# Kernel tuning notes

Hardware: AMD Instinct MI355X
Metric: run time of the kernel (lower is better)

The kernel has to match this reference:

```python
import jax, jax.numpy as jnp
import numpy as np

B, S, T, H, NH, G, E, I, R, L = 256, 256, 16, 1024, 8, 3, 8, 4096, 256, 3
GTEMP, RTEMP, TOPK_G, NEG = 1.0, 1.0, 2, -1e9

_W = {
    'ts_in_w': (3*H, H), 'ts_out_w': (H, H),
    'st_in_w': (3*H, H), 'st_out_w': (H, H),
    'ca_in_w': (3*H, H), 'ca_out_w': (H, H),
    'opq_w': (H, H), 'fuse_w': (H, 3*H), 'gate_w': (H, 3*H),
    'bs_w': (R, H), 'bt_w': (R, H), 'bo_w': (H, R),
    'cond_w': (H, 2*H), 'gr_w': (G, H), 'er_w': (G, E, H),
    'e_w1': (G, E, I, H), 'e_w2': (G, E, H, I), 'cls_w': (L, H),
}
_B = {
    'ts_in_b': (3*H,), 'ts_out_b': (H,), 'st_in_b': (3*H,), 'st_out_b': (H,),
    'ca_in_b': (3*H,), 'ca_out_b': (H,), 'fuse_b': (H,), 'gate_b': (H,),
    'bs_b': (R,), 'bt_b': (R,), 'bo_b': (H,), 'cond_b': (H,),
    'gr_b': (G,), 'er_b': (G, E), 'e_b1': (G, E, I), 'e_b2': (G, E, H),
    'cls_b': (L,), 'ln_b': (3*H,),
}


def setup_inputs() -> dict:
    key = jax.random.key(0)
    out = {}
    out['h_sent'] = jax.random.normal(jax.random.fold_in(key, 1), (B, S, H), dtype=jnp.float32)
    out['h_term'] = jax.random.normal(jax.random.fold_in(key, 2), (B, T, H), dtype=jnp.float32)
    for i, (name, shp) in enumerate(_W.items()):
        out[name] = 0.02 * jax.random.normal(jax.random.fold_in(key, 100 + i), shp, dtype=jnp.float32)
    for name, shp in _B.items():
        out[name] = jnp.zeros(shp, dtype=jnp.float32)
    out['ln_g'] = jnp.ones((3*H,), dtype=jnp.float32)
    return out


def _mha(q, k, v, w_in, b_in, w_out, b_out):
    # torch nn.MultiheadAttention (batch_first, eval mode / no dropout)
    wq, wk, wv = jnp.split(w_in, 3, axis=0)
    bq, bk, bv = jnp.split(b_in, 3, axis=0)
    Q, K, V = q @ wq.T + bq, k @ wk.T + bk, v @ wv.T + bv
    b, lq, _ = Q.shape
    lk = K.shape[1]
    d = H // NH
    Q = Q.reshape(b, lq, NH, d).transpose(0, 2, 1, 3)
    K = K.reshape(b, lk, NH, d).transpose(0, 2, 1, 3)
    V = V.reshape(b, lk, NH, d).transpose(0, 2, 1, 3)
    att = jax.nn.softmax(jnp.einsum('bhqd,bhkd->bhqk', Q, K) * (1.0 / d ** 0.5), axis=-1)
    o = jnp.einsum('bhqk,bhkd->bhqd', att, V).transpose(0, 2, 1, 3).reshape(b, lq, H)
    return o @ w_out.T + b_out


def _ln(x, g, b, eps=1e-5):
    mu = x.mean(-1, keepdims=True)
    var = ((x - mu) ** 2).mean(-1, keepdims=True)
    return (x - mu) * jax.lax.rsqrt(var + eps) * g + b


def reference(h_sent, h_term, ts_in_w, ts_in_b, ts_out_w, ts_out_b,
              st_in_w, st_in_b, st_out_w, st_out_b,
              ca_in_w, ca_in_b, ca_out_w, ca_out_b,
              opq_w, ln_g, ln_b, fuse_w, fuse_b, gate_w, gate_b,
              bs_w, bs_b, bt_w, bt_b, bo_w, bo_b, cond_w, cond_b,
              gr_w, gr_b, er_w, er_b, e_w1, e_b1, e_w2, e_b2, cls_w, cls_b):
    # --- co-attention fusion ---
    t2s = _mha(h_term, h_sent, h_sent, ts_in_w, ts_in_b, ts_out_w, ts_out_b)  # [B,T,H]
    s2t = _mha(h_sent, h_term, h_term, st_in_w, st_in_b, st_out_w, st_out_b)  # [B,S,H]
    v_term = t2s.mean(axis=1)   # [B,H]
    v_sent = s2t.mean(axis=1)   # [B,H]
    oq = h_term @ opq_w.T       # opinion query projection (no bias)
    v_op = _mha(oq, h_sent, h_sent, ca_in_w, ca_in_b, ca_out_w, ca_out_b).mean(axis=1)
    cat3 = jnp.concatenate([v_sent, v_term, v_op], axis=-1)        # [B,3H]
    fused_lin = _ln(cat3, ln_g, ln_b) @ fuse_w.T + fuse_b           # [B,H]
    g = jax.nn.sigmoid(cat3 @ gate_w.T + gate_b)                    # [B,H]
    bil = ((v_sent @ bs_w.T + bs_b) * (v_term @ bt_w.T + bt_b)) @ bo_w.T + bo_b
    fused = g * fused_lin + (1.0 - g) * bil                         # [B,H]
    cond = jnp.concatenate([fused, v_term], axis=-1) @ cond_w.T + cond_b  # [B,H]
    # --- hierarchical group -> expert soft routing ---
    glog = fused @ gr_w.T + gr_b                                    # [B,G]
    thr = jax.lax.top_k(glog, TOPK_G)[0][:, -1:]
    glog = jnp.where(glog >= thr, glog, NEG)
    gp = jax.nn.softmax(glog / GTEMP, axis=-1)                      # [B,G]
    elog = jnp.einsum('bh,geh->bge', cond, er_w) + er_b             # [B,G,E]
    ep = jax.nn.softmax(elog / RTEMP, axis=-1)
    # all experts applied densely (soft routing); FFN experts: GELU MLP
    h1 = jax.nn.gelu(jnp.einsum('bh,geih->bgei', fused, e_w1) + e_b1, approximate=False)
    y = jnp.einsum('bgei,gehi->bgeh', h1, e_w2) + e_b2              # [B,G,E,H]
    moe = jnp.einsum('bge,bgeh->bh', gp[:, :, None] * ep, y)
    out = fused + moe                                               # residual merge
    return out @ cls_w.T + cls_b                                    # [B,L]
```

## Files before the change

kernel.cpp:

```cpp
#include <hip/hip_runtime.h>
#include <math.h>


#define B_    256
#define S_    256
#define T_    16
#define H_    1024
#define NH_   8
#define DH_   128
#define M128_ 128
#define G_    3
#define E_    8
#define I_    4096
#define R_    256
#define L_    3
#define GE_   24

using bf16x8 = __attribute__((ext_vector_type(8))) __bf16;
using f32x4  = __attribute__((ext_vector_type(4))) float;

__device__ inline float wave_sum(float v) {
    for (int o = 32; o > 0; o >>= 1) v += __shfl_xor(v, o);
    return v;
}
__device__ inline float wave_max(float v) {
    for (int o = 32; o > 0; o >>= 1) v = fmaxf(v, __shfl_xor(v, o));
    return v;
}

__device__ inline void split8(const float4& f0, const float4& f1, bf16x8& hi, bf16x8& lo)
{
    const float fv[8] = {f0.x, f0.y, f0.z, f0.w, f1.x, f1.y, f1.z, f1.w};
#pragma unroll
    for (int j = 0; j < 8; ++j) {
        const __bf16 h = (__bf16)fv[j];
        hi[j] = h; lo[j] = (__bf16)(fv[j] - (float)h);
    }
}

__global__ __launch_bounds__(512) void fsc_k(
    const float* __restrict__ QALL, const float* __restrict__ wT3,
    const float* __restrict__ hs, const float* __restrict__ OFFS3,
    float* __restrict__ SC3, float rscale)
{
    const int zz = ((blockIdx.z & 7) << 7) | (blockIdx.z >> 3);
    const int b = zz >> 2, mod = zz & 3;
    if (mod == 3) return;

    __shared__ __bf16 A64h[128 * 72];
    __shared__ __bf16 A64l[128 * 72];
    __shared__ __bf16 Bh[128 * 40];
    __shared__ __bf16 Bl[128 * 40];

    const int tid  = threadIdx.x;
    const int lane = tid & 63;
    const int wid  = tid >> 6;
    const int fr   = lane & 15;
    const int fk   = lane >> 4;
    const int wm2  = (wid >> 2) * 64;
    const int wn2  = (wid & 3) * 32;

    bf16x8 qh[4], ql[4];
    {
        const float* qb = QALL + ((long)(b * 16 + fr)) * 4096 + mod * 1024 + wid * 128;
#pragma unroll
        for (int jc = 0; jc < 4; ++jc) {
            const float* p = qb + jc * 32 + fk * 8;
            split8(*(const float4*)p, *(const float4*)(p + 4), qh[jc], ql[jc]);
        }
    }

    f32x4 acc[2][4][2] = {};
    const float* wbase = wT3 + (long)mod * 1048576 + wid * 128;
    const float* hb = hs + (long)b * 262144;

    for (int ks = 0; ks < 16; ++ks) {
        __syncthreads();
#pragma unroll
        for (int nt = 0; nt < 4; ++nt) {
            f32x4 pa = {};
            const float* wr = wbase + (long)(ks * 64 + nt * 16 + fr) * 1024;
#pragma unroll
            for (int jc = 0; jc < 4; ++jc) {
                const float* p = wr + jc * 32 + fk * 8;
                bf16x8 wh, wl;
                split8(*(const float4*)p, *(const float4*)(p + 4), wh, wl);
                pa = __builtin_amdgcn_mfma_f32_16x16x32_bf16(qh[jc], wh, pa, 0, 0, 0);
                pa = __builtin_amdgcn_mfma_f32_16x16x32_bf16(qh[jc], wl, pa, 0, 0, 0);
                pa = __builtin_amdgcn_mfma_f32_16x16x32_bf16(ql[jc], wh, pa, 0, 0, 0);
            }
            const int kl = nt * 16 + fr;
#pragma unroll
            for (int r = 0; r < 4; ++r) {
                const int m = (fk * 4 + r) * 8 + wid;
                const float v = pa[r];
                const __bf16 hv = (__bf16)v;
                A64h[m * 72 + kl] = hv;
                A64l[m * 72 + kl] = (__bf16)(v - (float)hv);
            }
        }
#pragma unroll
        for (int half = 0; half < 2; ++half) {
#pragma unroll
            for (int kc = 0; kc < 2; ++kc) {
                __syncthreads();
                {
                    const int r2 = tid >> 2, q2 = tid & 3;
                    const float* p = hb + (long)(half * 128 + r2) * 1024 +
                                     ks * 64 + kc * 32 + q2 * 8;
                    bf16x8 hh, hl;
                    split8(*(const float4*)p, *(const float4*)(p + 4), hh, hl);
                    *(bf16x8*)&Bh[r2 * 40 + q2 * 8] = hh;
                    *(bf16x8*)&Bl[r2 * 40 + q2 * 8] = hl;
                }
                __syncthreads();
                const int klo = kc * 32 + fk * 8;
#pragma unroll
                for (int mt = 0; mt < 4; ++mt) {
                    const bf16x8 ah = *(const bf16x8*)&A64h[(wm2 + mt * 16 + fr) * 72 + klo];
                    const bf16x8 al = *(const bf16x8*)&A64l[(wm2 + mt * 16 + fr) * 72 + klo];
#pragma unroll
                    for (int nt = 0; nt < 2; ++nt) {
                        const bf16x8 bh = *(const bf16x8*)&Bh[(wn2 + nt * 16 + fr) * 40 + fk * 8];
                        const bf16x8 bl = *(const bf16x8*)&Bl[(wn2 + nt * 16 + fr) * 40 + fk * 8];
                        acc[half][mt][nt] = __builtin_amdgcn_mfma_f32_16x16x32_bf16(ah, bh, acc[half][mt][nt], 0, 0, 0);
                        acc[half][mt][nt] = __builtin_amdgcn_mfma_f32_16x16x32_bf16(ah, bl, acc[half][mt][nt], 0, 0, 0);
                        acc[half][mt][nt] = __builtin_amdgcn_mfma_f32_16x16x32_bf16(al, bh, acc[half][mt][nt], 0, 0, 0);
                    }
                }
            }
        }
    }

    float* out = SC3 + (long)mod * 8388608 + (long)b * 32768;
    const float* ro = OFFS3 + mod * 32768 + b * 128;
    const int lr4 = fk * 4;
#pragma unroll
    for (int half = 0; half < 2; ++half)
#pragma unroll
        for (int mt = 0; mt < 4; ++mt)
#pragma unroll
            for (int r = 0; r < 4; ++r) {
                const int rr = wm2 + mt * 16 + lr4 + r;
                const float rov = ro[rr];
#pragma unroll
                for (int nt = 0; nt < 2; ++nt) {
                    const int cc = half * 128 + wn2 + nt * 16 + fr;
                    out[(long)rr * 256 + cc] = (acc[half][mt][nt][r] + rov) * rscale;
                }
            }
}

template <int ACT>
__global__ __launch_bounds__(256) void sgemm2_k(
    const float* __restrict__ Ap, const float* __restrict__ Bp,
    const float* __restrict__ biasp, const float* __restrict__ roffp,
    float* __restrict__ Cf,
    int K, int m2shift, int zshift,
    long sA1, long sA2, long sAz1, long sAz2,
    long ldb, long sBz1, long sBz2, long sBia1, long sBia2,
    long sC1, long sC2, long sCz1, long sCz2, long sR1, long sR2,
    float scale)
{
    const int z  = blockIdx.z;
    const int z1 = z >> zshift;
    const int z2 = z & ((1 << zshift) - 1);
    const int m2mask = (1 << m2shift) - 1;
    const int row0 = blockIdx.y * 128;
    const int col0 = blockIdx.x * 128;
    const float* Ab = Ap + (long)z1 * sAz1 + (long)z2 * sAz2;
    const float* Bb = Bp + (long)z1 * sBz1 + (long)z2 * sBz2;
    const float* biasb = biasp ? biasp + (long)z1 * sBia1 + (long)z2 * sBia2 : nullptr;
    const float* roffb = roffp ? roffp + (long)z1 * sR1 + (long)z2 * sR2 : nullptr;

    __shared__ __bf16 Ahs[128 * 40];
    __shared__ __bf16 Als[128 * 40];
    __shared__ __bf16 Bhs[128 * 40];
    __shared__ __bf16 Bls[128 * 40];

    const int tid  = threadIdx.x;
    const int lane = tid & 63;
    const int wid  = tid >> 6;
    const int wm = (wid >> 1) * 64;
    const int wn = (wid & 1) * 64;
    const int fr  = lane & 15;
    const int fkb = (lane >> 4) * 16;
    const int qrow = tid >> 2;
    const int c4   = tid & 3;

    f32x4 acc[4][4] = {};
    float4 pfa[2][2], pfb[2][2];

    auto loadAB = [&](int k0) {
#pragma unroll
        for (int rep = 0; rep < 2; ++rep) {
            const int row = qrow + rep * 64;
            const int r = row0 + row;
            const int r1 = r >> m2shift, r2 = r & m2mask;
            const float* srcA = Ab + (long)r1 * sA1 + (long)r2 * sA2 + k0 + c4 * 8;
            pfa[rep][0] = *(const float4*)srcA;
            pfa[rep][1] = *(const float4*)(srcA + 4);
            const float* srcB = Bb + (long)(col0 + row) * ldb + k0 + c4 * 8;
            pfb[rep][0] = *(const float4*)srcB;
            pfb[rep][1] = *(const float4*)(srcB + 4);
        }
    };

    loadAB(0);
    for (int k0 = 0; k0 < K; k0 += 32) {
        __syncthreads();
#pragma unroll
        for (int rep = 0; rep < 2; ++rep) {
            const int row = qrow + rep * 64;
            bf16x8 hi, lo;
            split8(pfa[rep][0], pfa[rep][1], hi, lo);
            *(bf16x8*)&Ahs[row * 40 + c4 * 8] = hi;
            *(bf16x8*)&Als[row * 40 + c4 * 8] = lo;
            split8(pfb[rep][0], pfb[rep][1], hi, lo);
            *(bf16x8*)&Bhs[row * 40 + c4 * 8] = hi;
            *(bf16x8*)&Bls[row * 40 + c4 * 8] = lo;
        }
        __syncthreads();
        if (k0 + 32 < K) loadAB(k0 + 32);

        bf16x8 bh4[4], bl4[4];
#pragma unroll
        for (int n = 0; n < 4; ++n) {
            bh4[n] = *(const bf16x8*)((const char*)&Bhs[(wn + n * 16 + fr) * 40] + fkb);
            bl4[n] = *(const bf16x8*)((const char*)&Bls[(wn + n * 16 + fr) * 40] + fkb);
        }
#pragma unroll
        for (int m = 0; m < 4; ++m) {
            const bf16x8 ah = *(const bf16x8*)((const char*)&Ahs[(wm + m * 16 + fr) * 40] + fkb);
            const bf16x8 al = *(const bf16x8*)((const char*)&Als[(wm + m * 16 + fr) * 40] + fkb);
#pragma unroll
            for (int n = 0; n < 4; ++n) {
                acc[m][n] = __builtin_amdgcn_mfma_f32_16x16x32_bf16(ah, bh4[n], acc[m][n], 0, 0, 0);
                acc[m][n] = __builtin_amdgcn_mfma_f32_16x16x32_bf16(ah, bl4[n], acc[m][n], 0, 0, 0);
                acc[m][n] = __builtin_amdgcn_mfma_f32_16x16x32_bf16(al, bh4[n], acc[m][n], 0, 0, 0);
            }
        }
    }

    float* Cfb = Cf + (long)z1 * sCz1 + (long)z2 * sCz2;
    const int lr4 = (lane >> 4) * 4;
#pragma unroll
    for (int m = 0; m < 4; ++m) {
#pragma unroll
        for (int r = 0; r < 4; ++r) {
            const int rr = row0 + wm + m * 16 + lr4 + r;
            const int r1 = rr >> m2shift, r2 = rr & m2mask;
            const float ro = roffb ? roffb[rr] : 0.f;
            const long cb = (long)r1 * sC1 + (long)r2 * sC2;
#pragma unroll
            for (int n = 0; n < 4; ++n) {
                const int cc = col0 + wn + n * 16 + fr;
                float v = (acc[m][n][r] + ro) * scale;
                if (biasp) v += biasb[cc];
                if (ACT == 2) v = 1.0f / (1.0f + expf(-v));
                Cfb[cb + cc] = v;
            }
        }
    }
}

static void sg2(hipStream_t s, int act,
                const float* A, const float* B, const float* bias, const float* roff,
                float* C, int gx, int gy, int gz,
                int K, int m2shift, int zshift,
                long sA1, long sA2, long sAz1, long sAz2,
                long ldb, long sBz1, long sBz2, long sBia1, long sBia2,
                long sC1, long sC2, long sCz1, long sCz2, long sR1, long sR2,
                float scale)
{
    dim3 g(gx, gy, gz), b(256);
#define S2ARGS A, B, bias, roff, C, K, m2shift, zshift, sA1, sA2, sAz1, sAz2, \
               ldb, sBz1, sBz2, sBia1, sBia2, sC1, sC2, sCz1, sCz2, sR1, sR2, scale
    if (act == 2) sgemm2_k<2><<<g, b, 0, s>>>(S2ARGS);
    else          sgemm2_k<0><<<g, b, 0, s>>>(S2ARGS);
#undef S2ARGS
}

template <int ABF16, int BSING, int ACT, int WMUL, int OUTH>
__global__ __launch_bounds__(512) void sgemm256_k(
    const void* __restrict__ Ap, const float* __restrict__ Bp,
    const float* __restrict__ biasp, const float* __restrict__ wmulp,
    float* __restrict__ Cf, __bf16* __restrict__ Ch,
    int K, long sA1, long sAz, long ldb, long sBz, long sBz2, int bzshift,
    long sBias, long sC1, long sCz, long sWr, float scale)
{
    const int z    = blockIdx.z;
    const int col0 = blockIdx.x * 128;
    const int z1 = z >> bzshift;
    const int z2 = z - (z1 << bzshift);
    const float* Bb = Bp + (long)z1 * sBz + (long)z2 * sBz2;
    const float* biasb = biasp ? biasp + (long)z1 * sBias : nullptr;

    __shared__ __bf16 Ah[256 * 40];
    __shared__ __bf16 Al[ABF16 ? 64 : 256 * 40];
    __shared__ __bf16 Bh[128 * 40];
    __shared__ __bf16 Bl[BSING ? 64 : 128 * 40];

    const int tid  = threadIdx.x;
    const int lane = tid & 63;
    const int wid  = tid >> 6;
    const int wm = (wid >> 1) * 64;
    const int wn = (wid & 1) * 64;
    const int fr  = lane & 15;
    const int fkb = (lane >> 4) * 16;

    f32x4 acc[4][4] = {};
    bf16x8 pfah[2];
    float4 pfaf[2][2];
    float4 pfb[2];

    auto loadAB = [&](int k0) {
#pragma unroll
        for (int rep = 0; rep < 2; ++rep) {
            const int idx = tid + rep * 512;
            const int row = idx >> 2;
            const int cc4 = idx & 3;
            if (ABF16) {
                pfah[rep] = *(const bf16x8*)((const __bf16*)Ap + (long)z * sAz +
                                             (long)row * sA1 + k0 + cc4 * 8);
            } else {
                const float* src = (const float*)Ap + (long)z * sAz +
                                   (long)row * sA1 + k0 + cc4 * 8;
                pfaf[rep][0] = *(const float4*)src;
                pfaf[rep][1] = *(const float4*)(src + 4);
            }
        }
        {
            const int row = tid >> 2;
            const int cc4 = tid & 3;
            const float* src = Bb + (long)(col0 + row) * ldb + k0 + cc4 * 8;
            pfb[0] = *(const float4*)src;
            pfb[1] = *(const float4*)(src + 4);
        }
    };

    loadAB(0);
    for (int k0 = 0; k0 < K; k0 += 32) {
        __syncthreads();
#pragma unroll
        for (int rep = 0; rep < 2; ++rep) {
            const int idx = tid + rep * 512;
            const int row = idx >> 2;
            const int cc4 = idx & 3;
            if (ABF16) {
                *(bf16x8*)&Ah[row * 40 + cc4 * 8] = pfah[rep];
            } else {
                bf16x8 hi, lo;
                split8(pfaf[rep][0], pfaf[rep][1], hi, lo);
                *(bf16x8*)&Ah[row * 40 + cc4 * 8] = hi;
                *(bf16x8*)&Al[row * 40 + cc4 * 8] = lo;
            }
        }
        {
            const int row = tid >> 2;
            const int cc4 = tid & 3;
            bf16x8 hi, lo;
            split8(pfb[0], pfb[1], hi, lo);
            *(bf16x8*)&Bh[row * 40 + cc4 * 8] = hi;
            if (!BSING) *(bf16x8*)&Bl[row * 40 + cc4 * 8] = lo;
        }
        __syncthreads();
        if (k0 + 32 < K) loadAB(k0 + 32);

        bf16x8 bh4[4], bl4[4];
#pragma unroll
        for (int n = 0; n < 4; ++n) {
            bh4[n] = *(const bf16x8*)((const char*)&Bh[(wn + n * 16 + fr) * 40] + fkb);
            if (!BSING) bl4[n] = *(const bf16x8*)((const char*)&Bl[(wn + n * 16 + fr) * 40] + fkb);
        }
#pragma unroll
        for (int m = 0; m < 4; ++m) {
            const bf16x8 ah = *(const bf16x8*)((const char*)&Ah[(wm + m * 16 + fr) * 40] + fkb);
            bf16x8 al;
            if (!ABF16) al = *(const bf16x8*)((const char*)&Al[(wm + m * 16 + fr) * 40] + fkb);
#pragma unroll
            for (int n = 0; n < 4; ++n) {
                acc[m][n] = __builtin_amdgcn_mfma_f32_16x16x32_bf16(ah, bh4[n], acc[m][n], 0, 0, 0);
                if (!BSING) acc[m][n] = __builtin_amdgcn_mfma_f32_16x16x32_bf16(ah, bl4[n], acc[m][n], 0, 0, 0);
                if (!ABF16) acc[m][n] = __builtin_amdgcn_mfma_f32_16x16x32_bf16(al, bh4[n], acc[m][n], 0, 0, 0);
            }
        }
    }

    const int lr4 = (lane >> 4) * 4;
#pragma unroll
    for (int m = 0; m < 4; ++m) {
#pragma unroll
        for (int r = 0; r < 4; ++r) {
            const int rr = wm + m * 16 + lr4 + r;
#pragma unroll
            for (int n = 0; n < 4; ++n) {
                const int cc = col0 + wn + n * 16 + fr;
                float v = acc[m][n][r] * scale;
                if (biasp) v += biasb[cc];
                if (ACT == 1) v = 0.5f * v * (1.0f + erff(v * 0.70710678118654752f));
                if (WMUL) v *= wmulp[(long)rr * sWr + z];
                if (OUTH) Ch[(long)z * sCz + (long)rr * sC1 + cc] = (__bf16)v;
                else      Cf[(long)z * sCz + (long)rr * sC1 + cc] = v;
            }
        }
    }
}

__global__ void dotk_k(const float* __restrict__ A, const float* __restrict__ Bw,
                       const float* __restrict__ bias, float* __restrict__ out,
                       int MN, int N, int K)
{
    const int idx = blockIdx.x * (blockDim.x >> 6) + (threadIdx.x >> 6);
    if (idx >= MN) return;
    const int m = idx / N, n = idx - m * N;
    const int lane = threadIdx.x & 63;
    const float* a = A + (long)m * K;
    const float* bb = Bw + (long)n * K;
    float s = 0.f;
    for (int k = lane * 4; k < K; k += 256) {
        const float4 av = *(const float4*)(a + k);
        const float4 bv = *(const float4*)(bb + k);
        s += av.x * bv.x + av.y * bv.y + av.z * bv.z + av.w * bv.w;
    }
    s = wave_sum(s);
    if (lane == 0) out[idx] = s + (bias ? bias[n] : 0.f);
}

template <int ACT>
__global__ void kred_k(const float* __restrict__ part, const float* __restrict__ bias,
                       float* __restrict__ out, int n, long stride, int nz, int biasMask)
{
    const int i = blockIdx.x * blockDim.x + threadIdx.x;
    if (i >= n) return;
    float v = 0.f;
    for (int z = 0; z < nz; ++z) v += part[(long)z * stride + i];
    if (bias) v += bias[i & biasMask];
    if (ACT == 2) v = 1.0f / (1.0f + expf(-v));
    out[i] = v;
}

__global__ void cpy8_k(const float* s0, const float* s1, const float* s2, const float* s3,
                       const float* s4, const float* s5, const float* s6, const float* s7,
                       float* d0, float* d1, float* d2, float* d3,
                       float* d4, float* d5, float* d6, float* d7)
{
    const int seg = blockIdx.x >> 10;
    const int i = ((blockIdx.x & 1023) * 256 + threadIdx.x);
    const float* srcs[8] = {s0, s1, s2, s3, s4, s5, s6, s7};
    float* dsts[8] = {d0, d1, d2, d3, d4, d5, d6, d7};
    ((float4*)dsts[seg])[i] = ((const float4*)srcs[seg])[i];
}

__global__ void tT4_k(const float* s0, const float* s1, const float* s2, const float* s3,
                      float* d0, float* d1, float* d2, float* d3)
{
    __shared__ float t[32][33];
    const int seg = blockIdx.y >> 5;
    const float* src = seg == 0 ? s0 : seg == 1 ? s1 : seg == 2 ? s2 : s3;
    float* dst = seg == 0 ? d0 : seg == 1 ? d1 : seg == 2 ? d2 : d3;
    const int c0 = blockIdx.x * 32, r0 = (blockIdx.y & 31) * 32;
    const int tx = threadIdx.x & 31, ty = threadIdx.x >> 5;
#pragma unroll
    for (int i = 0; i < 4; ++i) {
        const int r = ty + i * 8;
        t[r][tx] = src[(long)(r0 + r) * 1024 + c0 + tx];
    }
    __syncthreads();
#pragma unroll
    for (int i = 0; i < 4; ++i) {
        const int r = ty + i * 8;
        dst[(long)(c0 + r) * 1024 + r0 + tx] = t[tx][r];
    }
}

__global__ void biascat_k(const float* __restrict__ ts_b, const float* __restrict__ ca_b,
                          const float* __restrict__ st_b,
                          const float* __restrict__ ts_ob, const float* __restrict__ ca_ob,
                          const float* __restrict__ st_ob,
                          float* __restrict__ BCAT, float* __restrict__ BKCAT,
                          float* __restrict__ WVB, float* __restrict__ WOB)
{
    const int i = blockIdx.x * blockDim.x + threadIdx.x;
    if (i >= 1024) return;
    BCAT[i] = ts_b[i]; BCAT[1024 + i] = ca_b[i];
    BCAT[2048 + i] = st_b[1024 + i]; BCAT[3072 + i] = st_b[2048 + i];
    BKCAT[i] = ts_b[1024 + i]; BKCAT[1024 + i] = ca_b[1024 + i]; BKCAT[2048 + i] = st_b[i];
    WVB[i] = ts_b[2048 + i]; WVB[1024 + i] = ca_b[2048 + i];
    WOB[i] = ts_ob[i]; WOB[1024 + i] = ca_ob[i]; WOB[2048 + i] = st_ob[i];
}

__global__ void headdot3_k(const float* __restrict__ QALL, const float* __restrict__ BKCAT,
                           float* __restrict__ out)
{
    const int idx = blockIdx.x * blockDim.x + threadIdx.x;
    if (idx >= 3 * B_ * T_ * NH_) return;
    const int mod = idx >> 15;
    const int b = (idx >> 7) & 255;
    const int t = (idx >> 3) & 15;
    const int h = idx & 7;
    const float* q = QALL + (long)(b * 16 + t) * 4096 + mod * 1024 + h * 128;
    const float* bb = BKCAT + mod * 1024 + h * 128;
    float sum = 0.f;
    for (int k = 0; k < DH_; ++k) sum += q[k] * bb[k];
    out[idx] = sum;
}

__global__ __launch_bounds__(64) void softpb_k(const float* __restrict__ sc3,
                                               float* __restrict__ pbar,
                                               float* __restrict__ attm)
{
    const int blk = blockIdx.x;
    const int h = blk & 7;
    const int b = (blk >> 3) & 255;
    const int mod = blk >> 11;
    const int lane = threadIdx.x;
    const float* base = sc3 + (long)mod * 8388608 + (long)b * 32768 + (long)h * 256;
    float v[16][4];
#pragma unroll
    for (int t = 0; t < 16; ++t) {
        const float* rowp = base + (long)t * 2048;
#pragma unroll
        for (int j = 0; j < 4; ++j) v[t][j] = rowp[j * 64 + lane];
    }
    if (mod < 2) {
        float pb[4] = {0.f, 0.f, 0.f, 0.f};
#pragma unroll
        for (int t = 0; t < 16; ++t) {
            float m = fmaxf(fmaxf(v[t][0], v[t][1]), fmaxf(v[t][2], v[t][3]));
            m = wave_max(m);
            const float e0 = expf(v[t][0] - m), e1 = expf(v[t][1] - m);
            const float e2 = expf(v[t][2] - m), e3 = expf(v[t][3] - m);
            const float inv = 1.f / wave_sum(e0 + e1 + e2 + e3);
            pb[0] += e0 * inv; pb[1] += e1 * inv; pb[2] += e2 * inv; pb[3] += e3 * inv;
        }
        float* pd = pbar + (long)mod * 524288 + (long)b * 2048 + h * 256;
#pragma unroll
        for (int j = 0; j < 4; ++j) pd[j * 64 + lane] = pb[j] * (1.0f / 16.f);
    } else {
        float am[16];
#pragma unroll
        for (int t = 0; t < 16; ++t) am[t] = 0.f;
#pragma unroll
        for (int j = 0; j < 4; ++j) {
            float mx = v[0][j];
#pragma unroll
            for (int t = 1; t < 16; ++t) mx = fmaxf(mx, v[t][j]);
            float e[16];
            float sum = 0.f;
#pragma unroll
            for (int t = 0; t < 16; ++t) { e[t] = expf(v[t][j] - mx); sum += e[t]; }
            const float inv = 1.f / sum;
#pragma unroll
            for (int t = 0; t < 16; ++t) am[t] += e[t] * inv;
        }
#pragma unroll
        for (int t = 0; t < 16; ++t) {
            const float sm = wave_sum(am[t]) * (1.0f / 256.f);
            if (lane == 0) attm[b * 128 + t * 8 + h] = sm;
        }
    }
}

__global__ __launch_bounds__(256) void ctxw2_k(const float* __restrict__ pbar,
                                               const float* __restrict__ hs,
                                               float* __restrict__ part)
{
    const int b = blockIdx.x;
    const int sc = blockIdx.y;
    __shared__ float pl[16][64];
    const int tid = threadIdx.x;
    for (int i = tid; i < 16 * 64; i += 256) {
        const int row = i >> 6;
        const int mod = row >> 3;
        pl[row][i & 63] = pbar[(long)mod * 524288 + (long)b * 2048 +
                               (row & 7) * 256 + sc * 64 + (i & 63)];
    }
    __syncthreads();
    const int k0 = tid * 4;
    float4 acc[16] = {};
    const float* hb = hs + (long)b * S_ * H_ + (long)sc * 64 * H_;
    for (int s = 0; s < 64; ++s) {
        const float4 vv = *(const float4*)(hb + (long)s * H_ + k0);
#pragma unroll
        for (int j = 0; j < 16; ++j) {
            const float p = pl[j][s];
            acc[j].x += p * vv.x; acc[j].y += p * vv.y;
            acc[j].z += p * vv.z; acc[j].w += p * vv.w;
        }
    }
    float* ob = part + (long)sc * 4194304;
#pragma unroll
    for (int j = 0; j < 16; ++j) {
        const int mod = j >> 3, hh = j & 7;
        *(float4*)(ob + (long)mod * 2097152 + (long)b * 8192 + hh * 1024 + k0) = acc[j];
    }
}

__global__ void ohead2_k(const float* __restrict__ attm, const float* __restrict__ QALL,
                         float* __restrict__ outb)
{
    const int idx = blockIdx.x * blockDim.x + threadIdx.x;
    if (idx >= B_ * H_) return;
    const int c = idx & (H_ - 1);
    const int b = idx >> 10;
    float sv = 0.f;
#pragma unroll
    for (int t = 0; t < T_; ++t)
        sv += attm[b * M128_ + t * NH_ + (c >> 7)] * QALL[(long)(b * 16 + t) * 4096 + 3072 + c];
    outb[idx] = sv;
}

__global__ void cat3_k(const float* __restrict__ vs, const float* __restrict__ vt,
                       const float* __restrict__ vo, float* __restrict__ out)
{
    const int idx = blockIdx.x * blockDim.x + threadIdx.x;
    if (idx >= B_ * 3 * H_) return;
    const int k = idx % (3 * H_);
    const int b = idx / (3 * H_);
    float v;
    if (k < H_)          v = vs[b * H_ + k];
    else if (k < 2 * H_) v = vt[b * H_ + k - H_];
    else                 v = vo[b * H_ + k - 2 * H_];
    out[idx] = v;
}

__global__ void ln_k(const float* __restrict__ cat3, const float* __restrict__ g,
                     const float* __restrict__ bta, float* __restrict__ out)
{
    const int b = blockIdx.x;
    const int tid = threadIdx.x;
    __shared__ float buf[3 * H_];
    __shared__ float red[4];
    const float* src = cat3 + (long)b * 3 * H_;
    float sv = 0.f;
    for (int i = tid; i < 3 * H_; i += 256) { const float x = src[i]; buf[i] = x; sv += x; }
    sv = wave_sum(sv);
    if ((tid & 63) == 0) red[tid >> 6] = sv;
    __syncthreads();
    const float mu = (red[0] + red[1] + red[2] + red[3]) * (1.f / (3 * H_));
    __syncthreads();
    float s2 = 0.f;
    for (int i = tid; i < 3 * H_; i += 256) { const float d0 = buf[i] - mu; s2 += d0 * d0; }
    s2 = wave_sum(s2);
    if ((tid & 63) == 0) red[tid >> 6] = s2;
    __syncthreads();
    const float var = (red[0] + red[1] + red[2] + red[3]) * (1.f / (3 * H_));
    const float rstd = rsqrtf(var + 1e-5f);
    float* dst = out + (long)b * 3 * H_;
    for (int i = tid; i < 3 * H_; i += 256)
        dst[i] = (buf[i] - mu) * rstd * g[i] + bta[i];
}

__global__ void mulf_k(const float* __restrict__ a, const float* __restrict__ b2,
                       float* __restrict__ out, int n)
{
    const int idx = blockIdx.x * blockDim.x + threadIdx.x;
    if (idx < n) out[idx] = a[idx] * b2[idx];
}

__global__ void fuse_k(const float* __restrict__ g, const float* __restrict__ flin,
                       const float* __restrict__ bil, float* __restrict__ fused,
                       __bf16* __restrict__ fusedh)
{
    const int idx = blockIdx.x * blockDim.x + threadIdx.x;
    if (idx >= B_ * H_) return;
    const float gg = g[idx];
    const float v = gg * flin[idx] + (1.f - gg) * bil[idx];
    fused[idx] = v;
    fusedh[idx] = (__bf16)v;
}

__global__ void catfv_k(const float* __restrict__ fused, const float* __restrict__ vt,
                        float* __restrict__ out)
{
    const int idx = blockIdx.x * blockDim.x + threadIdx.x;
    if (idx >= B_ * 2 * H_) return;
    const int k = idx % (2 * H_);
    const int b = idx / (2 * H_);
    out[idx] = (k < H_) ? fused[b * H_ + k] : vt[b * H_ + k - H_];
}

__global__ void route_k(const float* __restrict__ glog, float* __restrict__ gp)
{
    const int b = blockIdx.x * blockDim.x + threadIdx.x;
    if (b >= B_) return;
    const float x0 = glog[b * 3], x1 = glog[b * 3 + 1], x2 = glog[b * 3 + 2];
    const float m1 = fmaxf(x0, fmaxf(x1, x2));
    float thr;
    if (x0 == m1)      thr = fmaxf(x1, x2);
    else if (x1 == m1) thr = fmaxf(x0, x2);
    else               thr = fmaxf(x0, x1);
    const float y0 = (x0 >= thr) ? x0 : -1e9f;
    const float y1 = (x1 >= thr) ? x1 : -1e9f;
    const float y2 = (x2 >= thr) ? x2 : -1e9f;
    const float mm = fmaxf(y0, fmaxf(y1, y2));
    const float e0 = expf(y0 - mm), e1 = expf(y1 - mm), e2 = expf(y2 - mm);
    const float inv = 1.f / (e0 + e1 + e2);
    gp[b * 3] = e0 * inv; gp[b * 3 + 1] = e1 * inv; gp[b * 3 + 2] = e2 * inv;
}

__global__ void epsm_k(float* __restrict__ elog, const float* __restrict__ gp)
{
    const int idx = blockIdx.x * blockDim.x + threadIdx.x;
    if (idx >= B_ * G_) return;
    float* p = elog + (long)idx * E_;
    float m = p[0];
#pragma unroll
    for (int e = 1; e < E_; ++e) m = fmaxf(m, p[e]);
    float sum = 0.f;
    float v[E_];
#pragma unroll
    for (int e = 0; e < E_; ++e) { v[e] = expf(p[e] - m); sum += v[e]; }
    const float w = gp[idx] / sum;
#pragma unroll
    for (int e = 0; e < E_; ++e) p[e] = v[e] * w;
}

__global__ void moefinal_k(const float* __restrict__ part, const float* __restrict__ fused,
                           const float* __restrict__ wsc, const float* __restrict__ e_b2,
                           float* __restrict__ res)
{
    const int idx = blockIdx.x * blockDim.x + threadIdx.x;
    if (idx >= B_ * H_) return;
    const int b = idx >> 10;
    const int h = idx & (H_ - 1);
    float acc = fused[idx];
#pragma unroll 8
    for (int z = 0; z < 48; ++z) acc += part[(long)z * (B_ * H_) + idx];
    float ba = 0.f;
#pragma unroll
    for (int ge = 0; ge < GE_; ++ge) ba += wsc[b * GE_ + ge] * e_b2[ge * H_ + h];
    res[idx] = acc + ba;
}

extern "C" void kernel_launch(void* const* d_in, const int* in_sizes, int n_in,
                              void* d_out, int out_size, void* d_ws, size_t ws_size,
                              hipStream_t stream)
{
    const float* h_sent  = (const float*)d_in[0];
    const float* h_term  = (const float*)d_in[1];
    const float* ts_in_w = (const float*)d_in[2];
    const float* ts_out_w= (const float*)d_in[3];
    const float* st_in_w = (const float*)d_in[4];
    const float* st_out_w= (const float*)d_in[5];
    const float* ca_in_w = (const float*)d_in[6];
    const float* ca_out_w= (const float*)d_in[7];
    const float* opq_w   = (const float*)d_in[8];
    const float* fuse_w  = (const float*)d_in[9];
    const float* gate_w  = (const float*)d_in[10];
    const float* bs_w    = (const float*)d_in[11];
    const float* bt_w    = (const float*)d_in[12];
    const float* bo_w    = (const float*)d_in[13];
    const float* cond_w  = (const float*)d_in[14];
    const float* gr_w    = (const float*)d_in[15];
    const float* er_w    = (const float*)d_in[16];
    const float* e_w1    = (const float*)d_in[17];
    const float* e_w2    = (const float*)d_in[18];
    const float* cls_w   = (const float*)d_in[19];
    const float* ts_in_b = (const float*)d_in[20];
    const float* ts_out_b= (const float*)d_in[21];
    const float* st_in_b = (const float*)d_in[22];
    const float* st_out_b= (const float*)d_in[23];
    const float* ca_in_b = (const float*)d_in[24];
    const float* ca_out_b= (const float*)d_in[25];
    const float* fuse_b  = (const float*)d_in[26];
    const float* gate_b  = (const float*)d_in[27];
    const float* bs_b    = (const float*)d_in[28];
    const float* bt_b    = (const float*)d_in[29];
    const float* bo_b    = (const float*)d_in[30];
    const float* cond_b  = (const float*)d_in[31];
    const float* gr_b    = (const float*)d_in[32];
    const float* er_b    = (const float*)d_in[33];
    const float* e_b1    = (const float*)d_in[34];
    const float* e_b2    = (const float*)d_in[35];
    const float* cls_b   = (const float*)d_in[36];
    const float* ln_b    = (const float*)d_in[37];
    const float* ln_g    = (const float*)d_in[38];
    (void)in_sizes; (void)n_in; (void)out_size; (void)ws_size;

    float* ws = (float*)d_ws;
    size_t off = 0;
    auto allocF = [&](size_t n) { float* p = ws + off; off += (n + 63) & ~(size_t)63; return p; };

    float* QALL  = allocF(16777216);
    float* WCAT  = allocF(4194304);
    float* BCAT  = allocF(4096);
    float* BKCAT = allocF(3072);
    float* wT3   = allocF(3145728);
    float* opqT  = allocF(1048576);
    float* WVCAT = allocF(2097152);
    float* WVB   = allocF(2048);
    float* WOCAT = allocF(3145728);
    float* WOB   = allocF(3072);
    float* OFFS3 = allocF(98304);
    float* SC3   = allocF(25165824);
    float* PBAR3 = allocF(1048576);
    float* CTXB3 = allocF(4194304);
    float* PARTC = allocF(16777216);
    float* OBAR3 = allocF(786432);
    float* VOUT3 = allocF(786432);
    float* ATTM  = allocF(32768);
    float* CAT3  = allocF(786432);
    float* LNC   = allocF(786432);
    float* FLIN  = allocF(262144);
    float* GATE  = allocF(262144);
    float* BSV   = allocF(65536);
    float* BTV   = allocF(65536);
    float* PROD  = allocF(65536);
    float* BIL   = allocF(262144);
    float* FUSED = allocF(262144);
    float* FUSEDH= allocF(131072);
    float* CATFV = allocF(524288);
    float* COND  = allocF(262144);
    float* GLOG  = allocF(1024);
    float* GP    = allocF(1024);
    float* ELOG  = allocF(8192);
    float* RES   = allocF(262144);
    float* PARTF = allocF(1048576);
    float* H1Wf  = allocF(12582912);
    float* PART  = allocF(12582912);
    __bf16* FUSEDbf = (__bf16*)FUSEDH;
    __bf16* H1W     = (__bf16*)H1Wf;
    float* VTERM = VOUT3;
    float* VOP   = VOUT3 + 262144;
    float* VSENT = VOUT3 + 524288;

    hipStream_t s = stream;
    const float rscale = 0.08838834764831845f;

    cpy8_k<<<dim3(8 * 1024), dim3(256), 0, s>>>(
        ts_in_w, st_in_w + 1048576, st_in_w + 2097152, ts_in_w + 2097152,
        ca_in_w + 2097152, ts_out_w, ca_out_w, st_out_w,
        WCAT, WCAT + 2097152, WCAT + 3145728, WVCAT,
        WVCAT + 1048576, WOCAT, WOCAT + 1048576, WOCAT + 2097152);
    biascat_k<<<dim3(4), dim3(256), 0, s>>>(ts_in_b, ca_in_b, st_in_b,
                                            ts_out_b, ca_out_b, st_out_b,
                                            BCAT, BKCAT, WVB, WOB);
    tT4_k<<<dim3(32, 128), dim3(256), 0, s>>>(
        ts_in_w + 1048576, ca_in_w + 1048576, st_in_w, opq_w,
        wT3, wT3 + 1048576, wT3 + 2097152, opqT);

    sg2(s, 0, ca_in_w, opqT, nullptr, nullptr, WCAT + 1048576,
        8, 8, 1, 1024, 12, 0, 0, 1024, 0, 0, 1024, 0, 0, 0, 0,
        0, 1024, 0, 0, 0, 0, 1.f);

    sg2(s, 0, h_term, WCAT, BCAT, nullptr, QALL,
        32, 32, 1, 1024, 12, 0, 0, 1024, 0, 0, 1024, 0, 0, 0, 0,
        0, 4096, 0, 0, 0, 0, 1.f);

    headdot3_k<<<dim3(384), dim3(256), 0, s>>>(QALL, BKCAT, OFFS3);

    fsc_k<<<dim3(1, 1, 1024), dim3(512), 0, s>>>(QALL, wT3, h_sent, OFFS3, SC3, rscale);

    softpb_k<<<dim3(3 * B_ * NH_), dim3(64), 0, s>>>(SC3, PBAR3, ATTM);

    ctxw2_k<<<dim3(B_, 4), dim3(256), 0, s>>>(PBAR3, h_sent, PARTC);
    kred_k<0><<<dim3(4194304 / 256), dim3(256), 0, s>>>(PARTC, nullptr, CTXB3,
                                                        4194304, 4194304, 4, 0);
    sg2(s, 0, CTXB3, WVCAT, WVB, nullptr, OBAR3,
        1, 2, 16, 1024, 12, 3,
        0, 8192, 2097152, 1024,
        1024, 1048576, 131072, 1024, 128,
        0, 1024, 262144, 128, 0, 0, 1.f);

    ohead2_k<<<dim3((B_ * H_ + 255) / 256), dim3(256), 0, s>>>(ATTM, QALL, OBAR3 + 524288);

    sg2(s, 0, OBAR3, WOCAT, WOB, nullptr, VOUT3,
        8, 2, 3, 1024, 12, 0,
        0, 1024, 262144, 0,
        1024, 1048576, 0, 1024, 0,
        0, 1024, 262144, 0, 0, 0, 1.f);

    cat3_k<<<dim3((B_ * 3 * H_ + 255) / 256), dim3(256), 0, s>>>(VSENT, VTERM, VOP, CAT3);
    ln_k<<<dim3(B_), dim3(256), 0, s>>>(CAT3, ln_g, ln_b, LNC);
    sg2(s, 0, LNC, fuse_w, nullptr, nullptr, PARTF,
        8, 2, 4, 768, 12, 2, 0, 3072, 0, 768, 3072, 0, 768, 0, 0,
        0, 1024, 0, 262144, 0, 0, 1.f);
    kred_k<0><<<dim3(1024), dim3(256), 0, s>>>(PARTF, fuse_b, FLIN, 262144, 262144, 4, 1023);
    sg2(s, 0, CAT3, gate_w, nullptr, nullptr, PARTF,
        8, 2, 4, 768, 12, 2, 0, 3072, 0, 768, 3072, 0, 768, 0, 0,
        0, 1024, 0, 262144, 0, 0, 1.f);
    kred_k<2><<<dim3(1024), dim3(256), 0, s>>>(PARTF, gate_b, GATE, 262144, 262144, 4, 1023);
    sg2(s, 0, VSENT, bs_w, nullptr, nullptr, PARTF,
        2, 2, 4, 256, 12, 2, 0, 1024, 0, 256, 1024, 0, 256, 0, 0,
        0, 256, 0, 65536, 0, 0, 1.f);
    kred_k<0><<<dim3(256), dim3(256), 0, s>>>(PARTF, bs_b, BSV, 65536, 65536, 4, 255);
    sg2(s, 0, VTERM, bt_w, nullptr, nullptr, PARTF,
        2, 2, 4, 256, 12, 2, 0, 1024, 0, 256, 1024, 0, 256, 0, 0,
        0, 256, 0, 65536, 0, 0, 1.f);
    kred_k<0><<<dim3(256), dim3(256), 0, s>>>(PARTF, bt_b, BTV, 65536, 65536, 4, 255);
    mulf_k<<<dim3((B_ * R_ + 255) / 256), dim3(256), 0, s>>>(BSV, BTV, PROD, B_ * R_);
    sg2(s, 0, PROD, bo_w, nullptr, nullptr, PARTF,
        8, 2, 2, 128, 12, 1, 0, 256, 0, 128, 256, 0, 128, 0, 0,
        0, 1024, 0, 262144, 0, 0, 1.f);
    kred_k<0><<<dim3(1024), dim3(256), 0, s>>>(PARTF, bo_b, BIL, 262144, 262144, 2, 1023);
    fuse_k<<<dim3((B_ * H_ + 255) / 256), dim3(256), 0, s>>>(GATE, FLIN, BIL, FUSED, FUSEDbf);
    catfv_k<<<dim3((B_ * 2 * H_ + 255) / 256), dim3(256), 0, s>>>(FUSED, VTERM, CATFV);
    sg2(s, 0, CATFV, cond_w, nullptr, nullptr, PARTF,
        8, 2, 4, 512, 12, 2, 0, 2048, 0, 512, 2048, 0, 512, 0, 0,
        0, 1024, 0, 262144, 0, 0, 1.f);
    kred_k<0><<<dim3(1024), dim3(256), 0, s>>>(PARTF, cond_b, COND, 262144, 262144, 4, 1023);

    dotk_k<<<dim3(192), dim3(256), 0, s>>>(FUSED, gr_w, gr_b, GLOG, B_ * G_, G_, H_);
    route_k<<<dim3(1), dim3(256), 0, s>>>(GLOG, GP);
    dotk_k<<<dim3(1536), dim3(256), 0, s>>>(COND, er_w, er_b, ELOG, B_ * GE_, GE_, H_);
    epsm_k<<<dim3(3), dim3(256), 0, s>>>(ELOG, GP);

    sgemm256_k<1, 1, 1, 1, 1><<<dim3(I_ / 128, 1, GE_), dim3(512), 0, s>>>(
        FUSEDbf, e_w1, e_b1, ELOG, nullptr, H1W,
        1024, H_, 0, H_, (long)I_ * H_, 0, 0, I_,
        (long)GE_ * I_, I_, GE_, 1.f);
    sgemm256_k<1, 1, 0, 0, 0><<<dim3(H_ / 128, 1, 2 * GE_), dim3(512), 0, s>>>(
        H1W, e_w2, nullptr, nullptr, PART, nullptr,
        2048, (long)GE_ * I_, 2048, I_, (long)H_ * I_, 2048, 1, 0,
        H_, (long)B_ * H_, 0, 1.f);
    moefinal_k<<<dim3(B_ * H_ / 256), dim3(256), 0, s>>>(PART, FUSED, ELOG, e_b2, RES);

    dotk_k<<<dim3(192), dim3(256), 0, s>>>(RES, cls_w, cls_b, (float*)d_out, B_ * L_, L_, H_);
}
```

Baseline: 1.764 ms.

## Replace fused score kernel with two generic GEMMs through an intermediate buffer

Removes the fused fsc_k kernel, which projected queries through the key weights and multiplied by h_sent within one block using split-bf16 MFMA. It now runs two sgemm2 launches: the first writes per-head query-key products into a large BIG3 workspace, and the second multiplies that by h_sent with the offset and scale applied. This reuses the tuned generic GEMM and drops the awkward fused staging with its many barriers. In exchange it writes and re-reads an intermediate of roughly 400MB in global memory.

```diff
diff --git a/kernel.cpp b/kernel.cpp
--- a/kernel.cpp
+++ b/kernel.cpp
@@ -36,119 +36,6 @@
         const __bf16 h = (__bf16)fv[j];
         hi[j] = h; lo[j] = (__bf16)(fv[j] - (float)h);
     }
-}
-
-__global__ __launch_bounds__(512) void fsc_k(
-    const float* __restrict__ QALL, const float* __restrict__ wT3,
-    const float* __restrict__ hs, const float* __restrict__ OFFS3,
-    float* __restrict__ SC3, float rscale)
-{
-    const int zz = ((blockIdx.z & 7) << 7) | (blockIdx.z >> 3);
-    const int b = zz >> 2, mod = zz & 3;
-    if (mod == 3) return;
-
-    __shared__ __bf16 A64h[128 * 72];
-    __shared__ __bf16 A64l[128 * 72];
-    __shared__ __bf16 Bh[128 * 40];
-    __shared__ __bf16 Bl[128 * 40];
-
-    const int tid  = threadIdx.x;
-    const int lane = tid & 63;
-    const int wid  = tid >> 6;
-    const int fr   = lane & 15;
-    const int fk   = lane >> 4;
-    const int wm2  = (wid >> 2) * 64;
-    const int wn2  = (wid & 3) * 32;
-
-    bf16x8 qh[4], ql[4];
-    {
-        const float* qb = QALL + ((long)(b * 16 + fr)) * 4096 + mod * 1024 + wid * 128;
-#pragma unroll
-        for (int jc = 0; jc < 4; ++jc) {
-            const float* p = qb + jc * 32 + fk * 8;
-            split8(*(const float4*)p, *(const float4*)(p + 4), qh[jc], ql[jc]);
-        }
-    }
-
-    f32x4 acc[2][4][2] = {};
-    const float* wbase = wT3 + (long)mod * 1048576 + wid * 128;
-    const float* hb = hs + (long)b * 262144;
-
-    for (int ks = 0; ks < 16; ++ks) {
-        __syncthreads();
-#pragma unroll
-        for (int nt = 0; nt < 4; ++nt) {
-            f32x4 pa = {};
-            const float* wr = wbase + (long)(ks * 64 + nt * 16 + fr) * 1024;
-#pragma unroll
-            for (int jc = 0; jc < 4; ++jc) {
-                const float* p = wr + jc * 32 + fk * 8;
-                bf16x8 wh, wl;
-                split8(*(const float4*)p, *(const float4*)(p + 4), wh, wl);
-                pa = __builtin_amdgcn_mfma_f32_16x16x32_bf16(qh[jc], wh, pa, 0, 0, 0);
-                pa = __builtin_amdgcn_mfma_f32_16x16x32_bf16(qh[jc], wl, pa, 0, 0, 0);
-                pa = __builtin_amdgcn_mfma_f32_16x16x32_bf16(ql[jc], wh, pa, 0, 0, 0);
-            }
-            const int kl = nt * 16 + fr;
-#pragma unroll
-            for (int r = 0; r < 4; ++r) {
-                const int m = (fk * 4 + r) * 8 + wid;
-                const float v = pa[r];
-                const __bf16 hv = (__bf16)v;
-                A64h[m * 72 + kl] = hv;
-                A64l[m * 72 + kl] = (__bf16)(v - (float)hv);
-            }
-        }
-#pragma unroll
-        for (int half = 0; half < 2; ++half) {
-#pragma unroll
-            for (int kc = 0; kc < 2; ++kc) {
-                __syncthreads();
-                {
-                    const int r2 = tid >> 2, q2 = tid & 3;
-                    const float* p = hb + (long)(half * 128 + r2) * 1024 +
-                                     ks * 64 + kc * 32 + q2 * 8;
-                    bf16x8 hh, hl;
-                    split8(*(const float4*)p, *(const float4*)(p + 4), hh, hl);
-                    *(bf16x8*)&Bh[r2 * 40 + q2 * 8] = hh;
-                    *(bf16x8*)&Bl[r2 * 40 + q2 * 8] = hl;
-                }
-                __syncthreads();
-                const int klo = kc * 32 + fk * 8;
-#pragma unroll
-                for (int mt = 0; mt < 4; ++mt) {
-                    const bf16x8 ah = *(const bf16x8*)&A64h[(wm2 + mt * 16 + fr) * 72 + klo];
-                    const bf16x8 al = *(const bf16x8*)&A64l[(wm2 + mt * 16 + fr) * 72 + klo];
-#pragma unroll
-                    for (int nt = 0; nt < 2; ++nt) {
-                        const bf16x8 bh = *(const bf16x8*)&Bh[(wn2 + nt * 16 + fr) * 40 + fk * 8];
-                        const bf16x8 bl = *(const bf16x8*)&Bl[(wn2 + nt * 16 + fr) * 40 + fk * 8];
-                        acc[half][mt][nt] = __builtin_amdgcn_mfma_f32_16x16x32_bf16(ah, bh, acc[half][mt][nt], 0, 0, 0);
-                        acc[half][mt][nt] = __builtin_amdgcn_mfma_f32_16x16x32_bf16(ah, bl, acc[half][mt][nt], 0, 0, 0);
-                        acc[half][mt][nt] = __builtin_amdgcn_mfma_f32_16x16x32_bf16(al, bh, acc[half][mt][nt], 0, 0, 0);
-                    }
-                }
-            }
-        }
-    }
-
-    float* out = SC3 + (long)mod * 8388608 + (long)b * 32768;
-    const float* ro = OFFS3 + mod * 32768 + b * 128;
-    const int lr4 = fk * 4;
-#pragma unroll
-    for (int half = 0; half < 2; ++half)
-#pragma unroll
-        for (int mt = 0; mt < 4; ++mt)
-#pragma unroll
-            for (int r = 0; r < 4; ++r) {
-                const int rr = wm2 + mt * 16 + lr4 + r;
-                const float rov = ro[rr];
-#pragma unroll
-                for (int nt = 0; nt < 2; ++nt) {
-                    const int cc = half * 128 + wn2 + nt * 16 + fr;
-                    out[(long)rr * 256 + cc] = (acc[half][mt][nt][r] + rov) * rscale;
-                }
-            }
 }
 
 template <int ACT>
@@ -794,6 +681,7 @@
     float* WOCAT = allocF(3145728);
     float* WOB   = allocF(3072);
     float* OFFS3 = allocF(98304);
+    float* BIG3  = allocF(100663296);
     float* SC3   = allocF(25165824);
     float* PBAR3 = allocF(1048576);
     float* CTXB3 = allocF(4194304);
@@ -851,7 +739,17 @@
 
     headdot3_k<<<dim3(384), dim3(256), 0, s>>>(QALL, BKCAT, OFFS3);
 
-    fsc_k<<<dim3(1, 1, 1024), dim3(512), 0, s>>>(QALL, wT3, h_sent, OFFS3, SC3, rscale);
+    sg2(s, 0, QALL, wT3, nullptr, nullptr, BIG3,
+        8, 32, 24, 128, 4, 3,
+        65536, 4096, 1024, 128,
+        1024, 1048576, 128, 0, 0,
+        131072, 8192, 33554432, 1024, 0, 0, 1.f);
+
+    sg2(s, 0, BIG3, h_sent, nullptr, OFFS3, SC3,
+        2, 1, 768, 1024, 12, 8,
+        0, 1024, 33554432, 131072,
+        1024, 0, 262144, 0, 0,
+        0, 256, 8388608, 32768, 32768, 128, rscale);
 
     softpb_k<<<dim3(3 * B_ * NH_), dim3(64), 0, s>>>(SC3, PBAR3, ATTM);
 
```

Result: faster. 1.423 ms (-19.3%).
